# Performance work log

Hardware: AMD Instinct MI355X
Metric: run time of the kernel (lower is better)

## Reference

```python
import jax, jax.numpy as jnp
import numpy as np
from jax import lax

T = 1.0
B = 262144
STEPS = 20


def proj2manifold(x):
    # Polar-type retraction via SVD: nearest orthogonal matrix.
    u, _, vT = jnp.linalg.svd(x, full_matrices=False)
    return u @ vT


def setup_inputs() -> dict:
    key = jax.random.key(0)
    k1, k2, k3 = jax.random.split(key, 3)
    # Initial state: random matrices projected onto SO(3)/O(3).
    x0 = proj2manifold(jax.random.normal(k1, (B, 3, 3), dtype=jnp.float32))
    # Per-sample integration horizon t in (0, T].
    t = jax.random.uniform(k2, (B, 1), dtype=jnp.float32, minval=1e-3, maxval=T)
    # Pre-drawn Brownian increments (unit Gaussians), one per step.
    noise = jax.random.normal(k3, (STEPS, B, 3, 3), dtype=jnp.float32)
    return {"x": x0, "t": t, "noise": noise, "steps": STEPS}


def reference(x, t, noise, steps):
    # t: [B,1] -> [B,1,1]  (mirrors t.unsqueeze(2) in sample())
    dt = (t / steps)[:, :, None]           # [B,1,1]
    sqrt_dt = jnp.sqrt(dt)                 # [B,1,1]

    def step(xc, eps):
        inc = sqrt_dt * eps                # tangent-space Gaussian increment
        # proj2tangent: 0.5 * (v - x v^T x); drift f(x,t) = 0
        v = 0.5 * (inc - xc @ jnp.swapaxes(inc, -1, -2) @ xc)
        xn = proj2manifold(xc + v)         # SVD retraction back to manifold
        return xn, None

    xf, _ = lax.scan(step, x, noise)
    return xf
```

## Files before the change

kernel.cpp:

```cpp
#include <hip/hip_runtime.h>

#define TPB 256

__global__ __launch_bounds__(TPB) void brownian_so3_kernel(
    const float* __restrict__ x0,
    const float* __restrict__ t,
    const float* __restrict__ noise,
    float* __restrict__ out,
    int B, int steps)
{
    __shared__ float lds[2][TPB * 9];

    const int tid  = threadIdx.x;
    const int blk  = blockIdx.x;
    const long base = (long)blk * TPB * 9;
    const int b    = blk * TPB + tid;

    {
        const float4* src = (const float4*)(x0 + base);
        float4* dst = (float4*)lds[0];
        dst[tid]        = src[tid];
        dst[tid + TPB]  = src[tid + TPB];
        if (tid < 64) dst[tid + 2*TPB] = src[tid + 2*TPB];
    }
    __syncthreads();

    float x[9];
    #pragma unroll
    for (int j = 0; j < 9; ++j) x[j] = lds[0][tid*9 + j];
    __syncthreads();

    const float sd = sqrtf(t[b] / (float)steps);
    const float hs = 0.5f * sd;

    float4 r0, r1, r2 = make_float4(0.f, 0.f, 0.f, 0.f);
    {
        const float4* src = (const float4*)(noise + base);
        r0 = src[tid];
        r1 = src[tid + TPB];
        if (tid < 64) r2 = src[tid + 2*TPB];
    }

    for (int s = 0; s < steps; ++s) {
        float* buf = lds[s & 1];
        {
            float4* dst = (float4*)buf;
            dst[tid]       = r0;
            dst[tid + TPB] = r1;
            if (tid < 64) dst[tid + 2*TPB] = r2;
        }
        __syncthreads();

        if (s + 1 < steps) {
            const float4* src = (const float4*)(noise + (long)(s+1) * B * 9 + base);
            r0 = src[tid];
            r1 = src[tid + TPB];
            if (tid < 64) r2 = src[tid + 2*TPB];
        }

        float e[9];
        #pragma unroll
        for (int j = 0; j < 9; ++j) e[j] = buf[tid*9 + j];

        float wa = 0.f, wb = 0.f, wc = 0.f;
        #pragma unroll
        for (int k = 0; k < 3; ++k) {
            const float xk0 = x[k*3+0], xk1 = x[k*3+1], xk2 = x[k*3+2];
            const float ek0 = e[k*3+0], ek1 = e[k*3+1], ek2 = e[k*3+2];
            wa += xk2*ek1 - xk1*ek2;
            wb += xk0*ek2 - xk2*ek0;
            wc += xk1*ek0 - xk0*ek1;
        }
        const float A  = hs * wa;
        const float Bv = hs * wb;
        const float Cv = hs * wc;

        const float th2 = A*A + Bv*Bv + Cv*Cv;
        const float c1  = rsqrtf(1.0f + th2);
        const float c2  = c1*c1 / (1.0f + c1);

        const float q00 = 1.0f - c2*(Bv*Bv + Cv*Cv);
        const float q11 = 1.0f - c2*(A*A  + Cv*Cv);
        const float q22 = 1.0f - c2*(A*A  + Bv*Bv);
        const float q01 = c2*A*Bv  - c1*Cv;
        const float q10 = c2*A*Bv  + c1*Cv;
        const float q02 = c2*A*Cv  + c1*Bv;
        const float q20 = c2*A*Cv  - c1*Bv;
        const float q12 = c2*Bv*Cv - c1*A;
        const float q21 = c2*Bv*Cv + c1*A;

        #pragma unroll
        for (int r = 0; r < 3; ++r) {
            const float a0 = x[r*3+0], a1 = x[r*3+1], a2 = x[r*3+2];
            x[r*3+0] = a0*q00 + a1*q10 + a2*q20;
            x[r*3+1] = a0*q01 + a1*q11 + a2*q21;
            x[r*3+2] = a0*q02 + a1*q12 + a2*q22;
        }

        __syncthreads();
    }

    float* obuf = lds[0];
    #pragma unroll
    for (int j = 0; j < 9; ++j) obuf[tid*9 + j] = x[j];
    __syncthreads();
    {
        float4* dst = (float4*)(out + base);
        const float4* src = (const float4*)obuf;
        dst[tid]       = src[tid];
        dst[tid + TPB] = src[tid + TPB];
        if (tid < 64) dst[tid + 2*TPB] = src[tid + 2*TPB];
    }
}

extern "C" void kernel_launch(void* const* d_in, const int* in_sizes, int n_in,
                              void* d_out, int out_size, void* d_ws, size_t ws_size,
                              hipStream_t stream) {
    const float* x0    = (const float*)d_in[0];
    const float* t     = (const float*)d_in[1];
    const float* noise = (const float*)d_in[2];
    float* out = (float*)d_out;

    const int B     = in_sizes[0] / 9;
    const int steps = in_sizes[2] / in_sizes[0];

    const int grid = B / TPB;
    brownian_so3_kernel<<<grid, TPB, 0, stream>>>(x0, t, noise, out, B, steps);
}
```

Before: 37.88 us.

## Drop LDS staging and load noise per thread with two-step register prefetch

Replaces the block-cooperative float4 loads staged through shared memory with direct per-thread loads of each 3x3 matrix, using 4-byte-aligned vector loads. Noise is prefetched two steps ahead in registers, and the final result is written with nontemporal stores. This removes the per-step __syncthreads and the LDS round trips. In exchange, wave-level loads are no longer naturally 16-byte aligned and coalesced, which may split memory transactions in a kernel that is dominated by streaming the noise tensor.

```diff
diff --git a/kernel.cpp b/kernel.cpp
--- a/kernel.cpp
+++ b/kernel.cpp
@@ -1,6 +1,54 @@
 #include <hip/hip_runtime.h>
 
 #define TPB 256
+typedef float v4fa __attribute__((ext_vector_type(4), aligned(4)));
+
+#define NTS(v, p)  __builtin_nontemporal_store((v), (p))
+
+__device__ __forceinline__ void so3_step(float x[9], const float e[9], float hs) {
+    float wa = 0.f, wb = 0.f, wc = 0.f;
+    #pragma unroll
+    for (int k = 0; k < 3; ++k) {
+        const float xk0 = x[k*3+0], xk1 = x[k*3+1], xk2 = x[k*3+2];
+        const float ek0 = e[k*3+0], ek1 = e[k*3+1], ek2 = e[k*3+2];
+        wa += xk2*ek1 - xk1*ek2;
+        wb += xk0*ek2 - xk2*ek0;
+        wc += xk1*ek0 - xk0*ek1;
+    }
+    const float A  = hs * wa;
+    const float Bv = hs * wb;
+    const float Cv = hs * wc;
+
+    const float th2 = A*A + Bv*Bv + Cv*Cv;
+    const float c1  = rsqrtf(1.0f + th2);
+    const float c2  = c1*c1 / (1.0f + c1);
+
+    const float q00 = 1.0f - c2*(Bv*Bv + Cv*Cv);
+    const float q11 = 1.0f - c2*(A*A  + Cv*Cv);
+    const float q22 = 1.0f - c2*(A*A  + Bv*Bv);
+    const float q01 = c2*A*Bv  - c1*Cv;
+    const float q10 = c2*A*Bv  + c1*Cv;
+    const float q02 = c2*A*Cv  + c1*Bv;
+    const float q20 = c2*A*Cv  - c1*Bv;
+    const float q12 = c2*Bv*Cv - c1*A;
+    const float q21 = c2*Bv*Cv + c1*A;
+
+    #pragma unroll
+    for (int r = 0; r < 3; ++r) {
+        const float a0 = x[r*3+0], a1 = x[r*3+1], a2 = x[r*3+2];
+        x[r*3+0] = a0*q00 + a1*q10 + a2*q20;
+        x[r*3+1] = a0*q01 + a1*q11 + a2*q21;
+        x[r*3+2] = a0*q02 + a1*q12 + a2*q22;
+    }
+}
+
+__device__ __forceinline__ void load9(const float* __restrict__ p, float e[9]) {
+    v4fa lo = *(const v4fa*)(p);
+    v4fa hi = *(const v4fa*)(p + 4);
+    e[0] = lo.x; e[1] = lo.y; e[2] = lo.z; e[3] = lo.w;
+    e[4] = hi.x; e[5] = hi.y; e[6] = hi.z; e[7] = hi.w;
+    e[8] = p[8];
+}
 
 __global__ __launch_bounds__(TPB) void brownian_so3_kernel(
     const float* __restrict__ x0,
@@ -9,108 +57,41 @@
     float* __restrict__ out,
     int B, int steps)
 {
-    __shared__ float lds[2][TPB * 9];
+    const int b = blockIdx.x * TPB + threadIdx.x;
 
-    const int tid  = threadIdx.x;
-    const int blk  = blockIdx.x;
-    const long base = (long)blk * TPB * 9;
-    const int b    = blk * TPB + tid;
-
-    {
-        const float4* src = (const float4*)(x0 + base);
-        float4* dst = (float4*)lds[0];
-        dst[tid]        = src[tid];
-        dst[tid + TPB]  = src[tid + TPB];
-        if (tid < 64) dst[tid + 2*TPB] = src[tid + 2*TPB];
-    }
-    __syncthreads();
+    const float tv = t[b];
 
     float x[9];
-    #pragma unroll
-    for (int j = 0; j < 9; ++j) x[j] = lds[0][tid*9 + j];
-    __syncthreads();
+    load9(x0 + (long)b * 9, x);
 
-    const float sd = sqrtf(t[b] / (float)steps);
-    const float hs = 0.5f * sd;
+    const long stride = (long)B * 9;
+    const float* np = noise + (long)b * 9;
 
-    float4 r0, r1, r2 = make_float4(0.f, 0.f, 0.f, 0.f);
-    {
-        const float4* src = (const float4*)(noise + base);
-        r0 = src[tid];
-        r1 = src[tid + TPB];
-        if (tid < 64) r2 = src[tid + 2*TPB];
+    float cur[9], nxt[9];
+    load9(np, cur);
+    if (steps > 1) load9(np + stride, nxt);
+
+    const float hs = 0.5f * sqrtf(tv / (float)steps);
+
+    for (int s = 0; s < steps; ++s) {
+        float e[9];
+        #pragma unroll
+        for (int j = 0; j < 9; ++j) e[j] = cur[j];
+        #pragma unroll
+        for (int j = 0; j < 9; ++j) cur[j] = nxt[j];
+        if (s + 2 < steps) load9(np + (long)(s + 2) * stride, cur);
+        so3_step(x, e, hs);
+        #pragma unroll
+        for (int j = 0; j < 9; ++j) { float tmp = cur[j]; cur[j] = nxt[j]; nxt[j] = tmp; }
     }
 
-    for (int s = 0; s < steps; ++s) {
-        float* buf = lds[s & 1];
-        {
-            float4* dst = (float4*)buf;
-            dst[tid]       = r0;
-            dst[tid + TPB] = r1;
-            if (tid < 64) dst[tid + 2*TPB] = r2;
-        }
-        __syncthreads();
-
-        if (s + 1 < steps) {
-            const float4* src = (const float4*)(noise + (long)(s+1) * B * 9 + base);
-            r0 = src[tid];
-            r1 = src[tid + TPB];
-            if (tid < 64) r2 = src[tid + 2*TPB];
-        }
-
-        float e[9];
-        #pragma unroll
-        for (int j = 0; j < 9; ++j) e[j] = buf[tid*9 + j];
-
-        float wa = 0.f, wb = 0.f, wc = 0.f;
-        #pragma unroll
-        for (int k = 0; k < 3; ++k) {
-            const float xk0 = x[k*3+0], xk1 = x[k*3+1], xk2 = x[k*3+2];
-            const float ek0 = e[k*3+0], ek1 = e[k*3+1], ek2 = e[k*3+2];
-            wa += xk2*ek1 - xk1*ek2;
-            wb += xk0*ek2 - xk2*ek0;
-            wc += xk1*ek0 - xk0*ek1;
-        }
-        const float A  = hs * wa;
-        const float Bv = hs * wb;
-        const float Cv = hs * wc;
-
-        const float th2 = A*A + Bv*Bv + Cv*Cv;
-        const float c1  = rsqrtf(1.0f + th2);
-        const float c2  = c1*c1 / (1.0f + c1);
-
-        const float q00 = 1.0f - c2*(Bv*Bv + Cv*Cv);
-        const float q11 = 1.0f - c2*(A*A  + Cv*Cv);
-        const float q22 = 1.0f - c2*(A*A  + Bv*Bv);
-        const float q01 = c2*A*Bv  - c1*Cv;
-        const float q10 = c2*A*Bv  + c1*Cv;
-        const float q02 = c2*A*Cv  + c1*Bv;
-        const float q20 = c2*A*Cv  - c1*Bv;
-        const float q12 = c2*Bv*Cv - c1*A;
-        const float q21 = c2*Bv*Cv + c1*A;
-
-        #pragma unroll
-        for (int r = 0; r < 3; ++r) {
-            const float a0 = x[r*3+0], a1 = x[r*3+1], a2 = x[r*3+2];
-            x[r*3+0] = a0*q00 + a1*q10 + a2*q20;
-            x[r*3+1] = a0*q01 + a1*q11 + a2*q21;
-            x[r*3+2] = a0*q02 + a1*q12 + a2*q22;
-        }
-
-        __syncthreads();
-    }
-
-    float* obuf = lds[0];
-    #pragma unroll
-    for (int j = 0; j < 9; ++j) obuf[tid*9 + j] = x[j];
-    __syncthreads();
-    {
-        float4* dst = (float4*)(out + base);
-        const float4* src = (const float4*)obuf;
-        dst[tid]       = src[tid];
-        dst[tid + TPB] = src[tid + TPB];
-        if (tid < 64) dst[tid + 2*TPB] = src[tid + 2*TPB];
-    }
+    float* op = out + (long)b * 9;
+    v4fa lo, hi;
+    lo.x = x[0]; lo.y = x[1]; lo.z = x[2]; lo.w = x[3];
+    hi.x = x[4]; hi.y = x[5]; hi.z = x[6]; hi.w = x[7];
+    NTS(lo, (v4fa*)op);
+    NTS(hi, (v4fa*)(op + 4));
+    NTS(x[8], op + 8);
 }
 
 extern "C" void kernel_launch(void* const* d_in, const int* in_sizes, int n_in,
```

Result: no change. 37.69 us (-0.5%).
